# Kernel optimization log

Hardware: AMD Instinct MI355X
Metric: run time of the kernel (lower is better)

Reference implementation:

```python
import jax, jax.numpy as jnp
import numpy as np

B, CIN, COUT, ATOM = 128, 32, 128, 64
ITER_NUM = 5


def setup_inputs() -> dict:
    key = jax.random.key(0)
    x = jax.random.normal(key, (B, CIN, COUT, ATOM), dtype=jnp.float32)
    gamma = jnp.ones((1, CIN, 1, 1), dtype=jnp.float32)
    beta = jnp.zeros((1, CIN, 1, 1), dtype=jnp.float32)
    return {"x": x, "gamma": gamma, "beta": beta}


def _iter_norm_inv_sqrt(sigma, iter_num):
    # Newton-Schulz iterative inverse square root (IterNorm).
    trace = jnp.trace(sigma)
    sigma_n = sigma / trace  # trace-normalized so ||I - sigma_n|| < 1
    p = jnp.eye(sigma.shape[0], dtype=sigma.dtype)
    for _ in range(iter_num):
        p = 0.5 * (3.0 * p - p @ p @ p @ sigma_n)
    return p * jax.lax.rsqrt(trace)


def reference(x, gamma, beta):
    # x: [B, caps_in, caps_out, atom]; center per caps_in over (batch, caps_out, atom)
    mean = jnp.mean(x, axis=(0, 2, 3), keepdims=True)
    centered = x - mean
    norm_dim = COUT * ATOM * B
    # [B, caps_out, atom, caps_in] -> [N, caps_in]
    c = jnp.transpose(centered, (0, 2, 3, 1)).reshape(-1, CIN)
    sigma = (c.T @ c) / (jnp.float32(norm_dim) - 1.0)  # [caps_in, caps_in]
    inv_sqrt = _iter_norm_inv_sqrt(sigma, ITER_NUM)
    d = c @ inv_sqrt
    d = d.reshape(-1, COUT, ATOM, CIN)
    d = jnp.transpose(d, (0, 3, 1, 2))  # back to [B, caps_in, caps_out, atom]
    return d * gamma + beta
```

## Files before the change

### kernel.cpp

```cpp
#include <hip/hip_runtime.h>
#include <stdint.h>

constexpr int CIN  = 32;
constexpr int COLS_PER_B = 8192;
constexpr long long NTOT = 1048576;
constexpr float NTOTF = 1048576.0f;

typedef float f32x2 __attribute__((ext_vector_type(2)));

constexpr int PAD   = 260;
constexpr int GRID1 = 512;
constexpr int TPB   = 8;


__global__ __launch_bounds__(256) void stats_kernel(const float* __restrict__ x,
                                                    float* __restrict__ acc) {
    __shared__ float tile[2][CIN * PAD];
    __shared__ float ssum[CIN];
    const int t = threadIdx.x;
    const int w = t >> 6;
    const int l = t & 63;
    const int ti = l >> 3;
    const int tj = l & 7;

    float accg[4][4] = {};
    float asum[4] = {0.f, 0.f, 0.f, 0.f};
    if (t < CIN) ssum[t] = 0.f;

    const int tile0 = blockIdx.x * TPB;

    auto stage = [&](int buf, int tileid) {
        const int b = tileid >> 5;
        const int col0 = (tileid & 31) << 8;
        const float* base = x + (size_t)b * CIN * COLS_PER_B + col0 + l * 4;
        #pragma unroll
        for (int rr = 0; rr < 8; ++rr) {
            const int row = rr * 4 + w;
            const float* gp = base + (size_t)row * COLS_PER_B;
            __builtin_amdgcn_global_load_lds(
                (const __attribute__((address_space(1))) uint32_t*)gp,
                (__attribute__((address_space(3))) uint32_t*)&tile[buf][row * PAD],
                16, 0, 0);
        }
    };

    stage(0, tile0);
    __syncthreads();

    int buf = 0;
    for (int tt = 0; tt < TPB; ++tt) {
        if (tt + 1 < TPB) stage(buf ^ 1, tile0 + tt + 1);
        #pragma unroll
        for (int s = 0; s < 16; ++s) {
            const int k = w * 64 + s * 4;
            float4 av[4], bv[4];
            #pragma unroll
            for (int d = 0; d < 4; ++d) av[d] = *(const float4*)(&tile[buf][(ti + 8 * d) * PAD + k]);
            #pragma unroll
            for (int d = 0; d < 4; ++d) bv[d] = *(const float4*)(&tile[buf][(tj + 8 * d) * PAD + k]);
            #pragma unroll
            for (int di = 0; di < 4; ++di) {
                asum[di] += av[di].x + av[di].y + av[di].z + av[di].w;
                #pragma unroll
                for (int dj = 0; dj < 4; ++dj) {
                    accg[di][dj] += av[di].x * bv[dj].x + av[di].y * bv[dj].y
                                  + av[di].z * bv[dj].z + av[di].w * bv[dj].w;
                }
            }
        }
        __syncthreads();
        buf ^= 1;
    }

    float* flat = &tile[0][0];
    #pragma unroll
    for (int di = 0; di < 4; ++di)
        #pragma unroll
        for (int dj = 0; dj < 4; ++dj)
            flat[w * 1024 + (ti + 8 * di) * 32 + (tj + 8 * dj)] = accg[di][dj];
    if (tj == 0) {
        #pragma unroll
        for (int di = 0; di < 4; ++di) atomicAdd(&ssum[ti + 8 * di], asum[di]);
    }
    __syncthreads();
    #pragma unroll
    for (int q = 0; q < 4; ++q) {
        const int idx = t + q * 256;
        const float v = flat[idx] + flat[1024 + idx] + flat[2048 + idx] + flat[3072 + idx];
        atomicAdd(&acc[idx], v);
    }
    if (t < CIN) atomicAdd(&acc[1024 + t], ssum[t]);
}

__global__ __launch_bounds__(1024) void newton_kernel(const float* __restrict__ acc,
                                                      const float* __restrict__ gamma,
                                                      const float* __restrict__ beta,
                                                      float* __restrict__ outp) {
    __shared__ float sn[32 * 33], p[32 * 33], t1[32 * 33], t2[32 * 33];
    __shared__ float mean[32], diag[32], trs[1];
    const int t = threadIdx.x;
    const int i = t >> 5, j = t & 31;

    if (t < 32) mean[t] = acc[1024 + t] * (1.0f / NTOTF);
    __syncthreads();
    const float sig = (acc[t] - NTOTF * mean[i] * mean[j]) * (1.0f / (NTOTF - 1.0f));
    if (i == j) diag[i] = sig;
    __syncthreads();
    if (t == 0) {
        float tr = 0.f;
        for (int k = 0; k < 32; ++k) tr += diag[k];
        trs[0] = tr;
    }
    __syncthreads();
    const float tr = trs[0];
    sn[i * 33 + j] = sig / tr;
    p[i * 33 + j]  = (i == j) ? 1.0f : 0.0f;
    __syncthreads();

    for (int it = 0; it < 5; ++it) {
        float a = 0.f;
        #pragma unroll
        for (int k = 0; k < 32; ++k) a += p[i * 33 + k] * p[k * 33 + j];
        t1[i * 33 + j] = a;
        __syncthreads();
        float c = 0.f;
        #pragma unroll
        for (int k = 0; k < 32; ++k) c += t1[i * 33 + k] * p[k * 33 + j];
        t2[i * 33 + j] = c;
        __syncthreads();
        float v = 0.f;
        #pragma unroll
        for (int k = 0; k < 32; ++k) v += t2[i * 33 + k] * sn[k * 33 + j];
        const float pn = 1.5f * p[i * 33 + j] - 0.5f * v;
        __syncthreads();
        p[i * 33 + j] = pn;
        __syncthreads();
    }

    const float r = rsqrtf(tr);
    const float wv = p[i * 33 + j] * r * gamma[j];
    t1[i * 33 + j] = wv;
    outp[t] = wv;
    __syncthreads();
    if (t < 32) {
        float bb = beta[t];
        for (int k = 0; k < 32; ++k) bb -= mean[k] * t1[k * 33 + t];
        outp[1024 + t] = bb;
    }
}

__global__ __launch_bounds__(256, 4) void apply_kernel(const float* __restrict__ x,
                                                       const float* __restrict__ wm,
                                                       float* __restrict__ out) {
    const size_t tid  = (size_t)blockIdx.x * 256 + threadIdx.x;
    const size_t col2 = tid * 2;
    const size_t b    = col2 >> 13;
    const size_t c    = col2 & 8191;
    const float* xp = x + b * (size_t)(CIN * COLS_PER_B) + c;
    float* op       = out + b * (size_t)(CIN * COLS_PER_B) + c;

    float2 accv[32];
    #pragma unroll
    for (int j = 0; j < 32; ++j) {
        const float bv = wm[1024 + j];
        accv[j] = make_float2(bv, bv);
    }
    #pragma unroll
    for (int i = 0; i < 32; ++i) {
        const float2 v = *(const float2*)(xp + (size_t)i * COLS_PER_B);
        #pragma unroll
        for (int j = 0; j < 32; ++j) {
            const float sv = wm[i * 32 + j];
            accv[j].x += v.x * sv;
            accv[j].y += v.y * sv;
        }
    }
    #pragma unroll
    for (int j = 0; j < 32; ++j) {
        f32x2 v = { accv[j].x, accv[j].y };
        __builtin_nontemporal_store(v, (f32x2*)(op + (size_t)j * COLS_PER_B));
    }
}

extern "C" void kernel_launch(void* const* d_in, const int* in_sizes, int n_in,
                              void* d_out, int out_size, void* d_ws, size_t ws_size,
                              hipStream_t stream) {
    const float* x     = (const float*)d_in[0];
    const float* gamma = (const float*)d_in[1];
    const float* beta  = (const float*)d_in[2];
    float* out = (float*)d_out;
    float* acc = (float*)d_ws;

    (void)hipMemsetAsync(acc, 0, 1056 * sizeof(float), stream);
    stats_kernel<<<GRID1, 256, 0, stream>>>(x, acc);
    newton_kernel<<<1, 1024, 0, stream>>>(acc, gamma, beta, acc + 1056);
    apply_kernel<<<(NTOT / 2) / 256, 256, 0, stream>>>(x, acc + 1056, out);
}
```

Before: 389.5 us.

## Retile Gram stats kernel with 8x8 register blocks and 512 threads

The covariance kernel now uses 512 threads per block. Each lane computes an 8x8 register block of the Gram matrix over a strided k slice, and the partial sums are reduced across lanes with wave shuffles before going through LDS. The aim is a higher FMA-to-LDS-load ratio and fewer LDS reads per FLOP, at the cost of more registers per thread. The Newton iteration computes p@p and p@sn together, which drops one barrier per iteration by reassociating to (p@p)@(p@sn). The apply kernel reads its weights through a constant address-space pointer so they can be fetched as scalar loads.

```diff
diff --git a/kernel.cpp b/kernel.cpp
--- a/kernel.cpp
+++ b/kernel.cpp
@@ -8,23 +8,26 @@
 
 typedef float f32x2 __attribute__((ext_vector_type(2)));
 
-constexpr int PAD   = 260;
+constexpr int PADS  = 272;
 constexpr int GRID1 = 512;
 constexpr int TPB   = 8;
 
 
-__global__ __launch_bounds__(256) void stats_kernel(const float* __restrict__ x,
-                                                    float* __restrict__ acc) {
-    __shared__ float tile[2][CIN * PAD];
+__global__ __launch_bounds__(512, 4) void stats_kernel(const float* __restrict__ x,
+                                                       float* __restrict__ acc) {
+    __shared__ float tile[2][CIN][PADS];
     __shared__ float ssum[CIN];
-    const int t = threadIdx.x;
-    const int w = t >> 6;
-    const int l = t & 63;
-    const int ti = l >> 3;
-    const int tj = l & 7;
-
-    float accg[4][4] = {};
-    float asum[4] = {0.f, 0.f, 0.f, 0.f};
+    const int t   = threadIdx.x;
+    const int w   = t >> 6;
+    const int l   = t & 63;
+    const int kg  = l >> 4;
+    const int pos = l & 15;
+    const int pr  = pos >> 2;
+    const int pc  = pos & 3;
+    const int g   = w * 4 + kg;
+
+    float accg[8][8] = {};
+    float asum[8] = {};
     if (t < CIN) ssum[t] = 0.f;
 
     const int tile0 = blockIdx.x * TPB;
@@ -34,12 +37,12 @@
         const int col0 = (tileid & 31) << 8;
         const float* base = x + (size_t)b * CIN * COLS_PER_B + col0 + l * 4;
         #pragma unroll
-        for (int rr = 0; rr < 8; ++rr) {
-            const int row = rr * 4 + w;
+        for (int rr = 0; rr < 4; ++rr) {
+            const int row = w * 4 + rr;
             const float* gp = base + (size_t)row * COLS_PER_B;
             __builtin_amdgcn_global_load_lds(
                 (const __attribute__((address_space(1))) uint32_t*)gp,
-                (__attribute__((address_space(3))) uint32_t*)&tile[buf][row * PAD],
+                (__attribute__((address_space(3))) uint32_t*)&tile[buf][row][0],
                 16, 0, 0);
         }
     };
@@ -51,20 +54,19 @@
     for (int tt = 0; tt < TPB; ++tt) {
         if (tt + 1 < TPB) stage(buf ^ 1, tile0 + tt + 1);
         #pragma unroll
-        for (int s = 0; s < 16; ++s) {
-            const int k = w * 64 + s * 4;
-            float4 av[4], bv[4];
-            #pragma unroll
-            for (int d = 0; d < 4; ++d) av[d] = *(const float4*)(&tile[buf][(ti + 8 * d) * PAD + k]);
-            #pragma unroll
-            for (int d = 0; d < 4; ++d) bv[d] = *(const float4*)(&tile[buf][(tj + 8 * d) * PAD + k]);
-            #pragma unroll
-            for (int di = 0; di < 4; ++di) {
-                asum[di] += av[di].x + av[di].y + av[di].z + av[di].w;
+        for (int s = 0; s < 2; ++s) {
+            const int k0 = g * 4 + s * 128;
+            float4 bvv[8];
+            #pragma unroll
+            for (int e = 0; e < 8; ++e) bvv[e] = *(const float4*)&tile[buf][pc + 4 * e][k0];
+            #pragma unroll
+            for (int d = 0; d < 8; ++d) {
+                const float4 a = *(const float4*)&tile[buf][pr + 4 * d][k0];
+                asum[d] += a.x + a.y + a.z + a.w;
                 #pragma unroll
-                for (int dj = 0; dj < 4; ++dj) {
-                    accg[di][dj] += av[di].x * bv[dj].x + av[di].y * bv[dj].y
-                                  + av[di].z * bv[dj].z + av[di].w * bv[dj].w;
+                for (int e = 0; e < 8; ++e) {
+                    accg[d][e] += a.x * bvv[e].x + a.y * bvv[e].y
+                                + a.z * bvv[e].z + a.w * bvv[e].w;
                 }
             }
         }
@@ -72,21 +74,40 @@
         buf ^= 1;
     }
 
-    float* flat = &tile[0][0];
-    #pragma unroll
-    for (int di = 0; di < 4; ++di)
-        #pragma unroll
-        for (int dj = 0; dj < 4; ++dj)
-            flat[w * 1024 + (ti + 8 * di) * 32 + (tj + 8 * dj)] = accg[di][dj];
-    if (tj == 0) {
-        #pragma unroll
-        for (int di = 0; di < 4; ++di) atomicAdd(&ssum[ti + 8 * di], asum[di]);
-    }
-    __syncthreads();
-    #pragma unroll
-    for (int q = 0; q < 4; ++q) {
-        const int idx = t + q * 256;
-        const float v = flat[idx] + flat[1024 + idx] + flat[2048 + idx] + flat[3072 + idx];
+    #pragma unroll
+    for (int d = 0; d < 8; ++d) {
+        #pragma unroll
+        for (int e = 0; e < 8; ++e) {
+            float v = accg[d][e];
+            v += __shfl_xor(v, 16, 64);
+            v += __shfl_xor(v, 32, 64);
+            accg[d][e] = v;
+        }
+        float u = asum[d];
+        u += __shfl_xor(u, 16, 64);
+        u += __shfl_xor(u, 32, 64);
+        asum[d] = u;
+    }
+
+    float* flat = &tile[0][0][0];
+    if (kg == 0) {
+        #pragma unroll
+        for (int d = 0; d < 8; ++d)
+            #pragma unroll
+            for (int e = 0; e < 8; ++e)
+                flat[w * 1024 + (pr + 4 * d) * 32 + (pc + 4 * e)] = accg[d][e];
+        if (pc == 0) {
+            #pragma unroll
+            for (int d = 0; d < 8; ++d) atomicAdd(&ssum[pr + 4 * d], asum[d]);
+        }
+    }
+    __syncthreads();
+    #pragma unroll
+    for (int q = 0; q < 2; ++q) {
+        const int idx = t + q * 512;
+        float v = 0.f;
+        #pragma unroll
+        for (int ww = 0; ww < 8; ++ww) v += flat[ww * 1024 + idx];
         atomicAdd(&acc[idx], v);
     }
     if (t < CIN) atomicAdd(&acc[1024 + t], ssum[t]);
@@ -118,19 +139,19 @@
     __syncthreads();
 
     for (int it = 0; it < 5; ++it) {
-        float a = 0.f;
-        #pragma unroll
-        for (int k = 0; k < 32; ++k) a += p[i * 33 + k] * p[k * 33 + j];
+        float a = 0.f, c = 0.f;
+        #pragma unroll
+        for (int k = 0; k < 32; ++k) {
+            const float pik = p[i * 33 + k];
+            a += pik * p[k * 33 + j];
+            c += pik * sn[k * 33 + j];
+        }
         t1[i * 33 + j] = a;
-        __syncthreads();
-        float c = 0.f;
-        #pragma unroll
-        for (int k = 0; k < 32; ++k) c += t1[i * 33 + k] * p[k * 33 + j];
         t2[i * 33 + j] = c;
         __syncthreads();
         float v = 0.f;
         #pragma unroll
-        for (int k = 0; k < 32; ++k) v += t2[i * 33 + k] * sn[k * 33 + j];
+        for (int k = 0; k < 32; ++k) v += t1[i * 33 + k] * t2[k * 33 + j];
         const float pn = 1.5f * p[i * 33 + j] - 0.5f * v;
         __syncthreads();
         p[i * 33 + j] = pn;
@@ -149,9 +170,12 @@
     }
 }
 
+typedef const __attribute__((address_space(4))) float cfloat;
+
 __global__ __launch_bounds__(256, 4) void apply_kernel(const float* __restrict__ x,
-                                                       const float* __restrict__ wm,
+                                                       const float* __restrict__ wmp,
                                                        float* __restrict__ out) {
+    cfloat* wm = (cfloat*)wmp;
     const size_t tid  = (size_t)blockIdx.x * 256 + threadIdx.x;
     const size_t col2 = tid * 2;
     const size_t b    = col2 >> 13;
@@ -192,7 +216,7 @@
     float* acc = (float*)d_ws;
 
     (void)hipMemsetAsync(acc, 0, 1056 * sizeof(float), stream);
-    stats_kernel<<<GRID1, 256, 0, stream>>>(x, acc);
+    stats_kernel<<<GRID1, 512, 0, stream>>>(x, acc);
     newton_kernel<<<1, 1024, 0, stream>>>(acc, gamma, beta, acc + 1056);
     apply_kernel<<<(NTOT / 2) / 256, 256, 0, stream>>>(x, acc + 1056, out);
 }
```

Measured after the change: 493.6 us. +26.7%, slower.

## Swizzle stats LDS tiles, fuse Newton matmuls, read weights via constant address space

Applied to the files above, without the earlier changes.

The stats kernel now stages 128-column tiles with an XOR swizzle in place of padded 256-column tiles, and doubles the grid to 1024 blocks with an occupancy hint, to reduce LDS bank conflicts and raise occupancy. The Newton iteration is reassociated as (p·p)·(p·sn) so two products run in one loop, removing one barrier per iteration. The apply kernel reads the weight matrix through an address_space(4) pointer so the compiler can use scalar loads. The swizzle indexing must stay consistent between the global-to-LDS staging and the reads, which is easy to get wrong.

```diff
diff --git a/kernel.cpp b/kernel.cpp
--- a/kernel.cpp
+++ b/kernel.cpp
@@ -8,38 +8,39 @@
 
 typedef float f32x2 __attribute__((ext_vector_type(2)));
 
-constexpr int PAD   = 260;
-constexpr int GRID1 = 512;
+constexpr int TK    = 128;
+constexpr int GRID1 = 1024;
 constexpr int TPB   = 8;
 
 
-__global__ __launch_bounds__(256) void stats_kernel(const float* __restrict__ x,
-                                                    float* __restrict__ acc) {
-    __shared__ float tile[2][CIN * PAD];
+__global__ __launch_bounds__(256, 4) void stats_kernel(const float* __restrict__ x,
+                                                       float* __restrict__ acc) {
+    __shared__ float tile[2][CIN * TK];
     __shared__ float ssum[CIN];
-    const int t = threadIdx.x;
-    const int w = t >> 6;
-    const int l = t & 63;
+    const int t  = threadIdx.x;
+    const int w  = t >> 6;
+    const int l  = t & 63;
     const int ti = l >> 3;
     const int tj = l & 7;
 
     float accg[4][4] = {};
-    float asum[4] = {0.f, 0.f, 0.f, 0.f};
+    float asum[4] = {};
     if (t < CIN) ssum[t] = 0.f;
 
     const int tile0 = blockIdx.x * TPB;
 
     auto stage = [&](int buf, int tileid) {
-        const int b = tileid >> 5;
-        const int col0 = (tileid & 31) << 8;
-        const float* base = x + (size_t)b * CIN * COLS_PER_B + col0 + l * 4;
-        #pragma unroll
-        for (int rr = 0; rr < 8; ++rr) {
-            const int row = rr * 4 + w;
-            const float* gp = base + (size_t)row * COLS_PER_B;
+        const int b    = tileid >> 6;
+        const int col0 = (tileid & 63) << 7;
+        const float* base = x + (size_t)b * CIN * COLS_PER_B + col0;
+        #pragma unroll
+        for (int cc = 0; cc < 4; ++cc) {
+            const int row   = w * 8 + cc * 2 + (l >> 5);
+            const int chunk = (l & 31) ^ (row & 7);
+            const float* gp = base + (size_t)row * COLS_PER_B + chunk * 4;
             __builtin_amdgcn_global_load_lds(
                 (const __attribute__((address_space(1))) uint32_t*)gp,
-                (__attribute__((address_space(3))) uint32_t*)&tile[buf][row * PAD],
+                (__attribute__((address_space(3))) uint32_t*)&tile[buf][(w * 8 + cc * 2) * TK],
                 16, 0, 0);
         }
     };
@@ -51,20 +52,22 @@
     for (int tt = 0; tt < TPB; ++tt) {
         if (tt + 1 < TPB) stage(buf ^ 1, tile0 + tt + 1);
         #pragma unroll
-        for (int s = 0; s < 16; ++s) {
-            const int k = w * 64 + s * 4;
+        for (int s = 0; s < 8; ++s) {
+            const int k4 = w * 8 + s;
             float4 av[4], bv[4];
             #pragma unroll
-            for (int d = 0; d < 4; ++d) av[d] = *(const float4*)(&tile[buf][(ti + 8 * d) * PAD + k]);
+            for (int d = 0; d < 4; ++d)
+                av[d] = *(const float4*)&tile[buf][(ti + 8 * d) * TK + ((k4 ^ ti) << 2)];
             #pragma unroll
-            for (int d = 0; d < 4; ++d) bv[d] = *(const float4*)(&tile[buf][(tj + 8 * d) * PAD + k]);
+            for (int e = 0; e < 4; ++e)
+                bv[e] = *(const float4*)&tile[buf][(tj + 8 * e) * TK + ((k4 ^ tj) << 2)];
             #pragma unroll
-            for (int di = 0; di < 4; ++di) {
-                asum[di] += av[di].x + av[di].y + av[di].z + av[di].w;
+            for (int d = 0; d < 4; ++d) {
+                asum[d] += av[d].x + av[d].y + av[d].z + av[d].w;
                 #pragma unroll
-                for (int dj = 0; dj < 4; ++dj) {
-                    accg[di][dj] += av[di].x * bv[dj].x + av[di].y * bv[dj].y
-                                  + av[di].z * bv[dj].z + av[di].w * bv[dj].w;
+                for (int e = 0; e < 4; ++e) {
+                    accg[d][e] += av[d].x * bv[e].x + av[d].y * bv[e].y
+                                + av[d].z * bv[e].z + av[d].w * bv[e].w;
                 }
             }
         }
@@ -74,13 +77,13 @@
 
     float* flat = &tile[0][0];
     #pragma unroll
-    for (int di = 0; di < 4; ++di)
-        #pragma unroll
-        for (int dj = 0; dj < 4; ++dj)
-            flat[w * 1024 + (ti + 8 * di) * 32 + (tj + 8 * dj)] = accg[di][dj];
+    for (int d = 0; d < 4; ++d)
+        #pragma unroll
+        for (int e = 0; e < 4; ++e)
+            flat[w * 1024 + (ti + 8 * d) * 32 + (tj + 8 * e)] = accg[d][e];
     if (tj == 0) {
         #pragma unroll
-        for (int di = 0; di < 4; ++di) atomicAdd(&ssum[ti + 8 * di], asum[di]);
+        for (int d = 0; d < 4; ++d) atomicAdd(&ssum[ti + 8 * d], asum[d]);
     }
     __syncthreads();
     #pragma unroll
@@ -118,19 +121,19 @@
     __syncthreads();
 
     for (int it = 0; it < 5; ++it) {
-        float a = 0.f;
-        #pragma unroll
-        for (int k = 0; k < 32; ++k) a += p[i * 33 + k] * p[k * 33 + j];
+        float a = 0.f, c = 0.f;
+        #pragma unroll
+        for (int k = 0; k < 32; ++k) {
+            const float pik = p[i * 33 + k];
+            a += pik * p[k * 33 + j];
+            c += pik * sn[k * 33 + j];
+        }
         t1[i * 33 + j] = a;
-        __syncthreads();
-        float c = 0.f;
-        #pragma unroll
-        for (int k = 0; k < 32; ++k) c += t1[i * 33 + k] * p[k * 33 + j];
         t2[i * 33 + j] = c;
         __syncthreads();
         float v = 0.f;
         #pragma unroll
-        for (int k = 0; k < 32; ++k) v += t2[i * 33 + k] * sn[k * 33 + j];
+        for (int k = 0; k < 32; ++k) v += t1[i * 33 + k] * t2[k * 33 + j];
         const float pn = 1.5f * p[i * 33 + j] - 0.5f * v;
         __syncthreads();
         p[i * 33 + j] = pn;
@@ -149,9 +152,12 @@
     }
 }
 
+typedef const __attribute__((address_space(4))) float cfloat;
+
 __global__ __launch_bounds__(256, 4) void apply_kernel(const float* __restrict__ x,
-                                                       const float* __restrict__ wm,
+                                                       const float* __restrict__ wmp,
                                                        float* __restrict__ out) {
+    cfloat* wm = (cfloat*)wmp;
     const size_t tid  = (size_t)blockIdx.x * 256 + threadIdx.x;
     const size_t col2 = tid * 2;
     const size_t b    = col2 >> 13;
```

New measurement: 1.458 ms. 274% more time.
